# Optimization experiments

Hardware: AMD Instinct MI355X
Metric: run time of the kernel (lower is better)

The kernel has to match this reference:

```python
import jax, jax.numpy as jnp
import numpy as np

K = 9      # kernel_size
H = 6      # num_head
HD = 64    # head_dim
D = H * HD # reduced_hidden_dim = 384
B, S = 16, 1024
OUT = 384  # hidden_dim // 2


def setup_inputs() -> dict:
    key = jax.random.key(0)
    k = jax.random.split(key, 5)
    q = jax.random.normal(k[0], (B, S, D), dtype=jnp.float32)
    ks = jax.random.normal(k[1], (B, S, D), dtype=jnp.float32)
    v = jax.random.normal(k[2], (B, S, D), dtype=jnp.float32)
    Wk = jax.random.normal(k[3], (K * H, D), dtype=jnp.float32) * 0.02
    bk = jnp.zeros((K * H,), dtype=jnp.float32)
    Wp = jax.random.normal(k[4], (OUT, D), dtype=jnp.float32) * 0.02
    bp = jnp.zeros((OUT,), dtype=jnp.float32)
    return {"q": q, "ks": ks, "v": v, "Wk": Wk, "bk": bk, "Wp": Wp, "bp": bp}


def reference(q, ks, v, Wk, bk, Wp, bp):
    b, s, d = v.shape
    pad = K // 2
    # expand4conv: zero-pad along seq and gather K-wide sliding windows
    vp = jnp.pad(v, ((0, 0), (pad, pad), (0, 0)))            # [B, S+K-1, D]
    win = jnp.stack([vp[:, i:i + s] for i in range(K)], -1)  # [B, S, D, K]
    win = win.reshape(b, s, H, HD, K)                        # [B, S, H, HD, K]
    # dynamic kernel: softmax over kernel taps
    logits = jnp.einsum('bsd,od->bso', q * ks, Wk) + bk       # [B, S, K*H]
    dk = jax.nn.softmax(logits.reshape(b, s, H, K), axis=-1)  # [B, S, H, K]
    # local weighted reduction over the window
    out = jnp.einsum('bshdk,bshk->bshd', win, dk).reshape(b, s, d)
    return jnp.einsum('bsd,od->bso', out, Wp) + bp            # [B, S, OUT]
```

## Files before the change

### kernel.cpp

```cpp
#include <hip/hip_runtime.h>
#include <hip/hip_bf16.h>

#define BB 16
#define SS 1024
#define DD 384
#define HH 6
#define HDD 64
#define KK 9
#define KH 54
#define NP 64
#define OUTD 384
#define DKS 56

typedef __attribute__((ext_vector_type(4))) float floatx4;
typedef __attribute__((ext_vector_type(8))) __bf16 bf16x8;
typedef __attribute__((ext_vector_type(4))) __bf16 bf16x4;
typedef __attribute__((ext_vector_type(2))) __bf16 bf16x2;

__global__ __launch_bounds__(256) void cast_kernel(const float* __restrict__ Wk,
                                                   const float* __restrict__ Wp,
                                                   __bf16* __restrict__ WkB,
                                                   __bf16* __restrict__ WpB) {
    int i = blockIdx.x * 256 + threadIdx.x;
    if (i < NP * DD) {
        int r = i / DD;
        WkB[i] = (r < KH) ? (__bf16)Wk[i] : (__bf16)0.0f;
    } else {
        int j = i - NP * DD;
        if (j < OUTD * DD) WpB[j] = (__bf16)Wp[j];
    }
}

#define LBK 64
#define LLD 72

__global__ __launch_bounds__(256) void logits_kernel(const float* __restrict__ q,
                                                     const float* __restrict__ ks,
                                                     const __bf16* __restrict__ WkB,
                                                     const float* __restrict__ bk,
                                                     float* __restrict__ dkG) {
    __shared__ __bf16 qkS[64 * LLD];
    __shared__ __bf16 WkS[NP * LLD];
    __shared__ float  lgS[64 * 66];

    const int tid  = threadIdx.x;
    const int wave = tid >> 6;
    const int lane = tid & 63;
    const int m0   = blockIdx.x * 64;

    const int wm = wave * 16;
    const int fr = lane & 15;
    const int fk = (lane >> 4) * 8;

    floatx4 acc[4] = {};

    const int sr = tid >> 2;
    const int sc = (tid & 3) * 16;

    for (int k0 = 0; k0 < DD; k0 += LBK) {
        const float* qp = q  + (size_t)(m0 + sr) * DD + k0 + sc;
        const float* kp = ks + (size_t)(m0 + sr) * DD + k0 + sc;
#pragma unroll
        for (int c = 0; c < 16; c += 4) {
            floatx4 qv = *reinterpret_cast<const floatx4*>(qp + c);
            floatx4 kv = *reinterpret_cast<const floatx4*>(kp + c);
            floatx4 p = qv * kv;
            bf16x4 pk = { (__bf16)p.x, (__bf16)p.y, (__bf16)p.z, (__bf16)p.w };
            *reinterpret_cast<bf16x4*>(&qkS[sr * LLD + sc + c]) = pk;
        }
#pragma unroll
        for (int c = 0; c < 16; c += 8) {
            *reinterpret_cast<bf16x8*>(&WkS[sr * LLD + sc + c]) =
                *reinterpret_cast<const bf16x8*>(WkB + (size_t)sr * DD + k0 + sc + c);
        }
        __syncthreads();

#pragma unroll
        for (int kk = 0; kk < LBK; kk += 32) {
            bf16x8 afrag = *reinterpret_cast<const bf16x8*>(&qkS[(wm + fr) * LLD + kk + fk]);
#pragma unroll
            for (int j = 0; j < 4; ++j) {
                bf16x8 bfrag = *reinterpret_cast<const bf16x8*>(&WkS[(j * 16 + fr) * LLD + kk + fk]);
                acc[j] = __builtin_amdgcn_mfma_f32_16x16x32_bf16(afrag, bfrag, acc[j], 0, 0, 0);
            }
        }
        __syncthreads();
    }

    const int col_in = lane & 15;
    const int rgrp   = (lane >> 4) * 4;
#pragma unroll
    for (int j = 0; j < 4; ++j)
#pragma unroll
        for (int r = 0; r < 4; ++r)
            lgS[(wm + rgrp + r) * 66 + j * 16 + col_in] = acc[j][r];
    __syncthreads();

    for (int p = tid; p < 64 * HH; p += 256) {
        int row = p / HH, h = p % HH;
        float lg[KK];
        float mx = -1e30f;
#pragma unroll
        for (int k = 0; k < KK; ++k) {
            float s = lgS[row * 66 + h * KK + k] + bk[h * KK + k];
            lg[k] = s;
            mx = fmaxf(mx, s);
        }
        float sum = 0.0f;
#pragma unroll
        for (int k = 0; k < KK; ++k) { lg[k] = __expf(lg[k] - mx); sum += lg[k]; }
        float inv = 1.0f / sum;
        float* drow = dkG + (size_t)(m0 + row) * DKS + h * KK;
#pragma unroll
        for (int k = 0; k < KK; ++k) drow[k] = lg[k] * inv;
    }
}

#define CT 16

__global__ __launch_bounds__(256) void conv_kernel(const float* __restrict__ v,
                                                   const float* __restrict__ dkG,
                                                   __bf16* __restrict__ outA) {
    __shared__ float winS[(CT + 8) * DD];
    __shared__ float dkS[CT * DKS];

    const int blk = blockIdx.x;
    const int b   = blk / (SS / CT);
    const int s0  = (blk % (SS / CT)) * CT;
    const int tid = threadIdx.x;
    const size_t bs0 = (size_t)b * SS + s0;

    const float* vb = v + (size_t)b * SS * DD;
    for (int i = tid * 4; i < (CT + 8) * DD; i += 256 * 4) {
        int row = i / DD;
        int r = s0 - 4 + row;
        floatx4 val = {};
        if (r >= 0 && r < SS)
            val = *reinterpret_cast<const floatx4*>(vb + (size_t)r * DD + (i % DD));
        *reinterpret_cast<floatx4*>(&winS[i]) = val;
    }
    for (int j = tid; j < CT * DKS; j += 256) dkS[j] = dkG[bs0 * DKS + j];
    __syncthreads();

    const float2* win2 = reinterpret_cast<const float2*>(winS);
    for (int p = tid; p < CT * (DD / 2); p += 256) {
        int t = p / (DD / 2), dp = p % (DD / 2);
        int d = dp * 2, h = d >> 6;
        float ax = 0.0f, ay = 0.0f;
#pragma unroll
        for (int k = 0; k < KK; ++k) {
            float2 w = win2[(t + k) * (DD / 2) + dp];
            float dv = dkS[t * DKS + h * KK + k];
            ax += w.x * dv;
            ay += w.y * dv;
        }
        bf16x2 o = { (__bf16)ax, (__bf16)ay };
        *reinterpret_cast<bf16x2*>(&outA[(bs0 + t) * DD + d]) = o;
    }
}

#define BM 128
#define BN 64
#define BK 64
#define GLD 72

__global__ __launch_bounds__(256) void gemm_kernel(const __bf16* __restrict__ A,
                                                   const __bf16* __restrict__ Bw,
                                                   const float* __restrict__ bias,
                                                   float* __restrict__ Cout) {
    __shared__ __bf16 As[BM * GLD];
    __shared__ __bf16 Bs[BN * GLD];

    const int tid  = threadIdx.x;
    const int wave = tid >> 6;
    const int lane = tid & 63;

    const int mtile = blockIdx.x / (OUTD / BN);
    const int ntile = blockIdx.x % (OUTD / BN);
    const int m0 = mtile * BM;
    const int n0 = ntile * BN;

    const int wm = (wave >> 1) * 64;
    const int wn = (wave & 1) * 32;

    floatx4 acc[4][2] = {};

    const int fr = lane & 15;
    const int fk = (lane >> 4) * 8;

    for (int k0 = 0; k0 < DD; k0 += BK) {
#pragma unroll
        for (int p = 0; p < 4; ++p) {
            int idx = tid + p * 256;
            int r = idx >> 3, c = (idx & 7) * 8;
            *reinterpret_cast<bf16x8*>(&As[r * GLD + c]) =
                *reinterpret_cast<const bf16x8*>(A + (size_t)(m0 + r) * DD + k0 + c);
        }
#pragma unroll
        for (int p = 0; p < 2; ++p) {
            int idx = tid + p * 256;
            int r = idx >> 3, c = (idx & 7) * 8;
            *reinterpret_cast<bf16x8*>(&Bs[r * GLD + c]) =
                *reinterpret_cast<const bf16x8*>(Bw + (size_t)(n0 + r) * DD + k0 + c);
        }
        __syncthreads();

#pragma unroll
        for (int kk = 0; kk < BK; kk += 32) {
            bf16x8 bfrag[2];
#pragma unroll
            for (int j = 0; j < 2; ++j)
                bfrag[j] = *reinterpret_cast<const bf16x8*>(&Bs[(wn + j * 16 + fr) * GLD + kk + fk]);
#pragma unroll
            for (int i = 0; i < 4; ++i) {
                bf16x8 afrag = *reinterpret_cast<const bf16x8*>(&As[(wm + i * 16 + fr) * GLD + kk + fk]);
#pragma unroll
                for (int j = 0; j < 2; ++j)
                    acc[i][j] = __builtin_amdgcn_mfma_f32_16x16x32_bf16(afrag, bfrag[j], acc[i][j], 0, 0, 0);
            }
        }
        __syncthreads();
    }

    const int col_in = lane & 15;
    const int rgrp   = (lane >> 4) * 4;
#pragma unroll
    for (int i = 0; i < 4; ++i) {
#pragma unroll
        for (int j = 0; j < 2; ++j) {
            int col = n0 + wn + j * 16 + col_in;
            float bv = bias[col];
#pragma unroll
            for (int r = 0; r < 4; ++r) {
                int row = m0 + wm + i * 16 + rgrp + r;
                Cout[(size_t)row * OUTD + col] = acc[i][j][r] + bv;
            }
        }
    }
}

extern "C" void kernel_launch(void* const* d_in, const int* in_sizes, int n_in,
                              void* d_out, int out_size, void* d_ws, size_t ws_size,
                              hipStream_t stream) {
    const float* q  = (const float*)d_in[0];
    const float* ks = (const float*)d_in[1];
    const float* v  = (const float*)d_in[2];
    const float* Wk = (const float*)d_in[3];
    const float* bk = (const float*)d_in[4];
    const float* Wp = (const float*)d_in[5];
    const float* bp = (const float*)d_in[6];
    float* out = (float*)d_out;

    __bf16* WpB = (__bf16*)d_ws;
    __bf16* WkB = (__bf16*)((char*)d_ws + 294912);
    float*  dkG = (float*)((char*)d_ws + 294912 + 49152);
    __bf16* Abf = (__bf16*)((char*)d_ws + 294912 + 49152 + 3670016);

    cast_kernel<<<(NP * DD + OUTD * DD + 255) / 256, 256, 0, stream>>>(Wk, Wp, WkB, WpB);
    logits_kernel<<<(BB * SS) / 64, 256, 0, stream>>>(q, ks, WkB, bk, dkG);
    conv_kernel<<<(BB * SS) / CT, 256, 0, stream>>>(v, dkG, Abf);
    gemm_kernel<<<(BB * SS / BM) * (OUTD / BN), 256, 0, stream>>>(Abf, WpB, bp, out);
}
```

Measured before the change: 147.3 us.

## Fuse logits, softmax and dynamic conv into one kernel; restructure projection GEMM

Merges the logits GEMM, softmax and windowed convolution into a single kernel. The softmax weights stay in shared memory instead of making a round trip through global memory, and one launch is removed. The q*ks product is staged once across the full K dimension, Wk fragments are read directly from global memory, and v windows are read straight from global memory with a separate boundary path for edge tiles. The projection GEMM now holds the whole Wp tile in LDS and streams A fragments from global memory without per-k synchronisation, which trades LDS reuse of A for fewer barriers.

```diff
diff --git a/kernel.cpp b/kernel.cpp
--- a/kernel.cpp
+++ b/kernel.cpp
@@ -10,12 +10,12 @@
 #define KH 54
 #define NP 64
 #define OUTD 384
-#define DKS 56
 
 typedef __attribute__((ext_vector_type(4))) float floatx4;
 typedef __attribute__((ext_vector_type(8))) __bf16 bf16x8;
 typedef __attribute__((ext_vector_type(4))) __bf16 bf16x4;
-typedef __attribute__((ext_vector_type(2))) __bf16 bf16x2;
+
+#define QLD 392
 
 __global__ __launch_bounds__(256) void cast_kernel(const float* __restrict__ Wk,
                                                    const float* __restrict__ Wp,
@@ -31,60 +31,52 @@
     }
 }
 
-#define LBK 64
-#define LLD 72
-
-__global__ __launch_bounds__(256) void logits_kernel(const float* __restrict__ q,
-                                                     const float* __restrict__ ks,
-                                                     const __bf16* __restrict__ WkB,
-                                                     const float* __restrict__ bk,
-                                                     float* __restrict__ dkG) {
-    __shared__ __bf16 qkS[64 * LLD];
-    __shared__ __bf16 WkS[NP * LLD];
+__global__ __launch_bounds__(256) void fused_kernel(const float* __restrict__ q,
+                                                    const float* __restrict__ ks,
+                                                    const float* __restrict__ v,
+                                                    const __bf16* __restrict__ WkB,
+                                                    const float* __restrict__ bk,
+                                                    __bf16* __restrict__ outA) {
+    __shared__ __bf16 qkS[64 * QLD];
     __shared__ float  lgS[64 * 66];
 
     const int tid  = threadIdx.x;
     const int wave = tid >> 6;
     const int lane = tid & 63;
     const int m0   = blockIdx.x * 64;
+    const int b    = blockIdx.x >> 4;
+    const int s0   = (blockIdx.x & 15) * 64;
+
+    const int sr = tid >> 2;
+    const int sq = tid & 3;
+    {
+        const float* qp = q  + (size_t)(m0 + sr) * DD + sq * 4;
+        const float* kp = ks + (size_t)(m0 + sr) * DD + sq * 4;
+        __bf16* dst = &qkS[sr * QLD + sq * 4];
+#pragma unroll 6
+        for (int c = 0; c < 24; ++c) {
+            floatx4 qv = *reinterpret_cast<const floatx4*>(qp + c * 16);
+            floatx4 kv = *reinterpret_cast<const floatx4*>(kp + c * 16);
+            floatx4 pr = qv * kv;
+            bf16x4 pk = { (__bf16)pr.x, (__bf16)pr.y, (__bf16)pr.z, (__bf16)pr.w };
+            *reinterpret_cast<bf16x4*>(dst + c * 16) = pk;
+        }
+    }
+    __syncthreads();
 
     const int wm = wave * 16;
     const int fr = lane & 15;
     const int fk = (lane >> 4) * 8;
-
     floatx4 acc[4] = {};
-
-    const int sr = tid >> 2;
-    const int sc = (tid & 3) * 16;
-
-    for (int k0 = 0; k0 < DD; k0 += LBK) {
-        const float* qp = q  + (size_t)(m0 + sr) * DD + k0 + sc;
-        const float* kp = ks + (size_t)(m0 + sr) * DD + k0 + sc;
-#pragma unroll
-        for (int c = 0; c < 16; c += 4) {
-            floatx4 qv = *reinterpret_cast<const floatx4*>(qp + c);
-            floatx4 kv = *reinterpret_cast<const floatx4*>(kp + c);
-            floatx4 p = qv * kv;
-            bf16x4 pk = { (__bf16)p.x, (__bf16)p.y, (__bf16)p.z, (__bf16)p.w };
-            *reinterpret_cast<bf16x4*>(&qkS[sr * LLD + sc + c]) = pk;
-        }
-#pragma unroll
-        for (int c = 0; c < 16; c += 8) {
-            *reinterpret_cast<bf16x8*>(&WkS[sr * LLD + sc + c]) =
-                *reinterpret_cast<const bf16x8*>(WkB + (size_t)sr * DD + k0 + sc + c);
-        }
-        __syncthreads();
-
-#pragma unroll
-        for (int kk = 0; kk < LBK; kk += 32) {
-            bf16x8 afrag = *reinterpret_cast<const bf16x8*>(&qkS[(wm + fr) * LLD + kk + fk]);
-#pragma unroll
-            for (int j = 0; j < 4; ++j) {
-                bf16x8 bfrag = *reinterpret_cast<const bf16x8*>(&WkS[(j * 16 + fr) * LLD + kk + fk]);
-                acc[j] = __builtin_amdgcn_mfma_f32_16x16x32_bf16(afrag, bfrag, acc[j], 0, 0, 0);
-            }
-        }
-        __syncthreads();
+#pragma unroll 4
+    for (int kk = 0; kk < DD; kk += 32) {
+        bf16x8 afrag = *reinterpret_cast<const bf16x8*>(&qkS[(wm + fr) * QLD + kk + fk]);
+#pragma unroll
+        for (int j = 0; j < 4; ++j) {
+            bf16x8 bfrag = *reinterpret_cast<const bf16x8*>(
+                WkB + (size_t)(j * 16 + fr) * DD + kk + fk);
+            acc[j] = __builtin_amdgcn_mfma_f32_16x16x32_bf16(afrag, bfrag, acc[j], 0, 0, 0);
+        }
     }
 
     const int col_in = lane & 15;
@@ -96,139 +88,137 @@
             lgS[(wm + rgrp + r) * 66 + j * 16 + col_in] = acc[j][r];
     __syncthreads();
 
-    for (int p = tid; p < 64 * HH; p += 256) {
-        int row = p / HH, h = p % HH;
-        float lg[KK];
-        float mx = -1e30f;
-#pragma unroll
-        for (int k = 0; k < KK; ++k) {
-            float s = lgS[row * 66 + h * KK + k] + bk[h * KK + k];
-            lg[k] = s;
-            mx = fmaxf(mx, s);
-        }
-        float sum = 0.0f;
-#pragma unroll
-        for (int k = 0; k < KK; ++k) { lg[k] = __expf(lg[k] - mx); sum += lg[k]; }
-        float inv = 1.0f / sum;
-        float* drow = dkG + (size_t)(m0 + row) * DKS + h * KK;
-#pragma unroll
-        for (int k = 0; k < KK; ++k) drow[k] = lg[k] * inv;
-    }
-}
-
-#define CT 16
-
-__global__ __launch_bounds__(256) void conv_kernel(const float* __restrict__ v,
-                                                   const float* __restrict__ dkG,
-                                                   __bf16* __restrict__ outA) {
-    __shared__ float winS[(CT + 8) * DD];
-    __shared__ float dkS[CT * DKS];
-
-    const int blk = blockIdx.x;
-    const int b   = blk / (SS / CT);
-    const int s0  = (blk % (SS / CT)) * CT;
-    const int tid = threadIdx.x;
-    const size_t bs0 = (size_t)b * SS + s0;
+    float dkv[2][KK];
+#pragma unroll
+    for (int rr = 0; rr < 2; ++rr) {
+        int p = tid + rr * 256;
+        if (p < 64 * HH) {
+            int row = p / HH, h = p % HH;
+            float mx = -1e30f;
+#pragma unroll
+            for (int k = 0; k < KK; ++k) {
+                float s = lgS[row * 66 + h * KK + k] + bk[h * KK + k];
+                dkv[rr][k] = s;
+                mx = fmaxf(mx, s);
+            }
+            float sum = 0.0f;
+#pragma unroll
+            for (int k = 0; k < KK; ++k) { dkv[rr][k] = __expf(dkv[rr][k] - mx); sum += dkv[rr][k]; }
+            float inv = 1.0f / sum;
+#pragma unroll
+            for (int k = 0; k < KK; ++k) dkv[rr][k] *= inv;
+        }
+    }
+    __syncthreads();
+    float* dkS = lgS;
+#pragma unroll
+    for (int rr = 0; rr < 2; ++rr) {
+        int p = tid + rr * 256;
+        if (p < 64 * HH) {
+            int row = p / HH, h = p % HH;
+#pragma unroll
+            for (int k = 0; k < KK; ++k) dkS[row * 56 + h * KK + k] = dkv[rr][k];
+        }
+    }
+    __syncthreads();
 
     const float* vb = v + (size_t)b * SS * DD;
-    for (int i = tid * 4; i < (CT + 8) * DD; i += 256 * 4) {
-        int row = i / DD;
-        int r = s0 - 4 + row;
-        floatx4 val = {};
-        if (r >= 0 && r < SS)
-            val = *reinterpret_cast<const floatx4*>(vb + (size_t)r * DD + (i % DD));
-        *reinterpret_cast<floatx4*>(&winS[i]) = val;
-    }
-    for (int j = tid; j < CT * DKS; j += 256) dkS[j] = dkG[bs0 * DKS + j];
-    __syncthreads();
-
-    const float2* win2 = reinterpret_cast<const float2*>(winS);
-    for (int p = tid; p < CT * (DD / 2); p += 256) {
-        int t = p / (DD / 2), dp = p % (DD / 2);
-        int d = dp * 2, h = d >> 6;
-        float ax = 0.0f, ay = 0.0f;
-#pragma unroll
-        for (int k = 0; k < KK; ++k) {
-            float2 w = win2[(t + k) * (DD / 2) + dp];
-            float dv = dkS[t * DKS + h * KK + k];
-            ax += w.x * dv;
-            ay += w.y * dv;
-        }
-        bf16x2 o = { (__bf16)ax, (__bf16)ay };
-        *reinterpret_cast<bf16x2*>(&outA[(bs0 + t) * DD + d]) = o;
-    }
-}
-
-#define BM 128
-#define BN 64
-#define BK 64
-#define GLD 72
+    __bf16* ob = outA + (size_t)m0 * DD;
+    const bool edge = (s0 == 0) || (s0 == SS - 64);
+    if (!edge) {
+#pragma unroll 2
+        for (int it = 0; it < 24; ++it) {
+            int tt = it * 256 + tid;
+            int row = tt / 96, c4 = tt % 96;
+            int h = c4 >> 4;
+            const float* dkr = &dkS[row * 56 + h * KK];
+            const float* vp = vb + (size_t)(s0 + row - 4) * DD + c4 * 4;
+            floatx4 a = {};
+#pragma unroll
+            for (int k = 0; k < KK; ++k) {
+                floatx4 w = *reinterpret_cast<const floatx4*>(vp + (size_t)k * DD);
+                float dv = dkr[k];
+                a += w * dv;
+            }
+            bf16x4 o = { (__bf16)a.x, (__bf16)a.y, (__bf16)a.z, (__bf16)a.w };
+            *reinterpret_cast<bf16x4*>(&ob[(size_t)row * DD + c4 * 4]) = o;
+        }
+    } else {
+#pragma unroll 2
+        for (int it = 0; it < 24; ++it) {
+            int tt = it * 256 + tid;
+            int row = tt / 96, c4 = tt % 96;
+            int h = c4 >> 4;
+            const float* dkr = &dkS[row * 56 + h * KK];
+            floatx4 a = {};
+#pragma unroll
+            for (int k = 0; k < KK; ++k) {
+                int r = s0 + row - 4 + k;
+                floatx4 w = {};
+                if (r >= 0 && r < SS)
+                    w = *reinterpret_cast<const floatx4*>(vb + (size_t)r * DD + c4 * 4);
+                float dv = dkr[k];
+                a += w * dv;
+            }
+            bf16x4 o = { (__bf16)a.x, (__bf16)a.y, (__bf16)a.z, (__bf16)a.w };
+            *reinterpret_cast<bf16x4*>(&ob[(size_t)row * DD + c4 * 4]) = o;
+        }
+    }
+}
 
 __global__ __launch_bounds__(256) void gemm_kernel(const __bf16* __restrict__ A,
                                                    const __bf16* __restrict__ Bw,
                                                    const float* __restrict__ bias,
                                                    float* __restrict__ Cout) {
-    __shared__ __bf16 As[BM * GLD];
-    __shared__ __bf16 Bs[BN * GLD];
+    __shared__ __bf16 Bs[64 * QLD];
 
     const int tid  = threadIdx.x;
     const int wave = tid >> 6;
     const int lane = tid & 63;
 
-    const int mtile = blockIdx.x / (OUTD / BN);
-    const int ntile = blockIdx.x % (OUTD / BN);
-    const int m0 = mtile * BM;
-    const int n0 = ntile * BN;
-
-    const int wm = (wave >> 1) * 64;
-    const int wn = (wave & 1) * 32;
-
-    floatx4 acc[4][2] = {};
-
+    const int mtile = blockIdx.x / (OUTD / 64);
+    const int ntile = blockIdx.x % (OUTD / 64);
+    const int m0 = mtile * 128;
+    const int n0 = ntile * 64;
+
+#pragma unroll 4
+    for (int j = 0; j < 12; ++j) {
+        int id = tid + j * 256;
+        int r = id / 48, ch = (id % 48) * 8;
+        *reinterpret_cast<bf16x8*>(&Bs[r * QLD + ch]) =
+            *reinterpret_cast<const bf16x8*>(Bw + (size_t)(n0 + r) * DD + ch);
+    }
+    __syncthreads();
+
+    const int wm = wave * 32;
     const int fr = lane & 15;
     const int fk = (lane >> 4) * 8;
 
-    for (int k0 = 0; k0 < DD; k0 += BK) {
-#pragma unroll
-        for (int p = 0; p < 4; ++p) {
-            int idx = tid + p * 256;
-            int r = idx >> 3, c = (idx & 7) * 8;
-            *reinterpret_cast<bf16x8*>(&As[r * GLD + c]) =
-                *reinterpret_cast<const bf16x8*>(A + (size_t)(m0 + r) * DD + k0 + c);
-        }
-#pragma unroll
-        for (int p = 0; p < 2; ++p) {
-            int idx = tid + p * 256;
-            int r = idx >> 3, c = (idx & 7) * 8;
-            *reinterpret_cast<bf16x8*>(&Bs[r * GLD + c]) =
-                *reinterpret_cast<const bf16x8*>(Bw + (size_t)(n0 + r) * DD + k0 + c);
-        }
-        __syncthreads();
-
-#pragma unroll
-        for (int kk = 0; kk < BK; kk += 32) {
-            bf16x8 bfrag[2];
-#pragma unroll
-            for (int j = 0; j < 2; ++j)
-                bfrag[j] = *reinterpret_cast<const bf16x8*>(&Bs[(wn + j * 16 + fr) * GLD + kk + fk]);
-#pragma unroll
-            for (int i = 0; i < 4; ++i) {
-                bf16x8 afrag = *reinterpret_cast<const bf16x8*>(&As[(wm + i * 16 + fr) * GLD + kk + fk]);
-#pragma unroll
-                for (int j = 0; j < 2; ++j)
-                    acc[i][j] = __builtin_amdgcn_mfma_f32_16x16x32_bf16(afrag, bfrag[j], acc[i][j], 0, 0, 0);
-            }
-        }
-        __syncthreads();
+    floatx4 acc[2][4] = {};
+
+#pragma unroll 4
+    for (int kk = 0; kk < DD; kk += 32) {
+        bf16x8 afrag[2];
+#pragma unroll
+        for (int i = 0; i < 2; ++i)
+            afrag[i] = *reinterpret_cast<const bf16x8*>(
+                A + (size_t)(m0 + wm + i * 16 + fr) * DD + kk + fk);
+#pragma unroll
+        for (int j = 0; j < 4; ++j) {
+            bf16x8 bfrag = *reinterpret_cast<const bf16x8*>(&Bs[(j * 16 + fr) * QLD + kk + fk]);
+#pragma unroll
+            for (int i = 0; i < 2; ++i)
+                acc[i][j] = __builtin_amdgcn_mfma_f32_16x16x32_bf16(afrag[i], bfrag, acc[i][j], 0, 0, 0);
+        }
     }
 
     const int col_in = lane & 15;
     const int rgrp   = (lane >> 4) * 4;
 #pragma unroll
-    for (int i = 0; i < 4; ++i) {
-#pragma unroll
-        for (int j = 0; j < 2; ++j) {
-            int col = n0 + wn + j * 16 + col_in;
+    for (int i = 0; i < 2; ++i) {
+#pragma unroll
+        for (int j = 0; j < 4; ++j) {
+            int col = n0 + j * 16 + col_in;
             float bv = bias[col];
 #pragma unroll
             for (int r = 0; r < 4; ++r) {
@@ -253,11 +243,9 @@
 
     __bf16* WpB = (__bf16*)d_ws;
     __bf16* WkB = (__bf16*)((char*)d_ws + 294912);
-    float*  dkG = (float*)((char*)d_ws + 294912 + 49152);
-    __bf16* Abf = (__bf16*)((char*)d_ws + 294912 + 49152 + 3670016);
+    __bf16* Abf = (__bf16*)((char*)d_ws + 294912 + 49152);
 
     cast_kernel<<<(NP * DD + OUTD * DD + 255) / 256, 256, 0, stream>>>(Wk, Wp, WkB, WpB);
-    logits_kernel<<<(BB * SS) / 64, 256, 0, stream>>>(q, ks, WkB, bk, dkG);
-    conv_kernel<<<(BB * SS) / CT, 256, 0, stream>>>(v, dkG, Abf);
-    gemm_kernel<<<(BB * SS / BM) * (OUTD / BN), 256, 0, stream>>>(Abf, WpB, bp, out);
-}
+    fused_kernel<<<(BB * SS) / 64, 256, 0, stream>>>(q, ks, v, WkB, bk, Abf);
+    gemm_kernel<<<(BB * SS / 128) * (OUTD / 64), 256, 0, stream>>>(Abf, WpB, bp, out);
+}
```

Result: slower. 160.4 us (+8.9%).
